# Kernel optimization log

Hardware: AMD Instinct MI355X
Metric: run time of the kernel (lower is better)

The kernel has to match this reference:

```python
import math
import jax, jax.numpy as jnp
from jax import lax
import numpy as np

N_LAYERS = 16
MAX_DIL = 128
C_RES = 64
C_DIL = 128
ENC_F = 256
ENC_S = 256
LOOP = int(math.floor(math.log2(MAX_DIL))) + 1  # 8
DILS = [2 ** (i % LOOP) for i in range(N_LAYERS)]  # 1..128 twice


def setup_inputs() -> dict:
    key = jax.random.key(0)
    ks = jax.random.split(key, 9)
    B, T = 8, 131072
    signal = jax.random.normal(ks[0], (B, 1, T), dtype=jnp.float32)
    # params (xavier-ish scales ~ 1/sqrt(fan_in+fan_out))
    W0 = jax.random.normal(ks[1], (C_RES, 1), dtype=jnp.float32) * 0.5          # 1x1 input conv
    b0 = jax.random.normal(ks[2], (C_RES,), dtype=jnp.float32) * 0.02
    Wd = jax.random.normal(ks[3], (N_LAYERS, C_DIL, C_RES, 2), dtype=jnp.float32) * 0.08  # k=2 dilated convs
    bd = jax.random.normal(ks[4], (N_LAYERS, C_DIL), dtype=jnp.float32) * 0.02
    Wr = jax.random.normal(ks[5], (N_LAYERS, C_RES, C_DIL), dtype=jnp.float32) * 0.08     # 1x1 residual convs
    br = jax.random.normal(ks[6], (N_LAYERS, C_RES), dtype=jnp.float32) * 0.02
    Wf = jax.random.normal(ks[7], (1, C_RES), dtype=jnp.float32) * 0.1          # 1x1 final conv
    bf = jax.random.normal(ks[8], (1,), dtype=jnp.float32) * 0.02
    return {"signal": signal, "W0": W0, "b0": b0, "Wd": Wd, "bd": bd,
            "Wr": Wr, "br": br, "Wf": Wf, "bf": bf}


def reference(signal, W0, b0, Wd, bd, Wr, br, Wf, bf):
    # input 1x1 conv: [B,1,T] -> [B,C_RES,T]
    x = jnp.einsum('oi,bit->bot', W0, signal) + b0[None, :, None]
    for i, d in enumerate(DILS):
        skip = x
        h = jax.nn.relu(x)
        # kernel-2 dilated conv, VALID (no causal pad in original): len shrinks by d
        L = h.shape[2]
        h = (jnp.einsum('oc,bct->bot', Wd[i, :, :, 0], h[:, :, :L - d])
             + jnp.einsum('oc,bct->bot', Wd[i, :, :, 1], h[:, :, d:])
             + bd[i][None, :, None])
        h = jax.nn.relu(h)
        # 1x1 residual conv back to C_RES
        h = jnp.einsum('oc,bct->bot', Wr[i], h) + br[i][None, :, None]
        # residual add with right-aligned trim of skip
        x = h + skip[:, :, skip.shape[2] - h.shape[2]:]
    # final 1x1 conv -> [B,1,L']
    x = jnp.einsum('oc,bct->bot', Wf, x) + bf[None, :, None]
    # AvgPool1d(ENC_F, stride=ENC_S), VALID, count_include_pad irrelevant (no pad)
    x = lax.reduce_window(x, 0.0, lax.add, (1, 1, ENC_F), (1, 1, ENC_S), 'VALID') / ENC_F
    return x
```

## Files before the change

kernel.cpp:

```cpp
#include <hip/hip_runtime.h>
#include <hip/hip_bf16.h>
#include <stdint.h>

typedef __attribute__((ext_vector_type(8))) short short8;
typedef __attribute__((ext_vector_type(4))) float f32x4;
typedef unsigned short bfu;

#define T_TILE  128
#define RING    384
#define NLAYERS 16
#define T0LEN   131072
#define BATCH   8
#define RFIELD  510
#define FINLEN  130560
#define CHCAP   65280

#define BARRIER() asm volatile("s_waitcnt lgkmcnt(0)\n\ts_barrier" ::: "memory")

__device__ __forceinline__ bfu f2bf(float f) {
    unsigned u = __float_as_uint(f);
    u += 0x7FFFu + ((u >> 16) & 1u);
    return (bfu)(u >> 16);
}
__device__ __forceinline__ unsigned pk2(float a, float b) {
    __hip_bfloat16 lo = __float2bfloat16(a);
    __hip_bfloat16 hi = __float2bfloat16(b);
    unsigned short ul = __builtin_bit_cast(unsigned short, lo);
    unsigned short uh = __builtin_bit_cast(unsigned short, hi);
    return (unsigned)ul | ((unsigned)uh << 16);
}
__device__ __forceinline__ float bf2f(bfu h) { return __uint_as_float(((unsigned)h) << 16); }
__device__ __forceinline__ unsigned relu2(unsigned w) {
    return w & ~(((w >> 15) & 0x00010001u) * 0xFFFFu);
}

__global__ void prep_weights(const float* __restrict__ Wd, const float* __restrict__ Wr,
                             bfu* __restrict__ wcat, bfu* __restrict__ wrb)
{
    int idx = blockIdx.x * 256 + threadIdx.x;
    const int total1 = NLAYERS * 128 * 128;
    if (idx < total1) {
        int k = idx & 127, o = (idx >> 7) & 127, l = idx >> 14;
        int tap = k >> 6, c = k & 63;
        wcat[idx] = f2bf(Wd[(((l * 128 + o) * 64) + c) * 2 + tap]);
    } else {
        int j = idx - total1;
        if (j < NLAYERS * 64 * 128) wrb[j] = f2bf(Wr[j]);
    }
}

template <int MODE>
__global__ __launch_bounds__(256, 2)
void layer_kernel(const bfu* __restrict__ xin, bfu* __restrict__ xout,
                  const bfu* __restrict__ wcat, const bfu* __restrict__ wrb,
                  const float* __restrict__ bd, const float* __restrict__ br,
                  const float* __restrict__ sig, const float* __restrict__ W0,
                  const float* __restrict__ b0, const float* __restrict__ Wf,
                  float* __restrict__ partial,
                  int s, int d, int Lin, int Lout, int Rrows, int NT, int tiles)
{
    __shared__ bfu rx[RING * 64];
    __shared__ bfu hb[128 * 128];

    const int tid  = threadIdx.x;
    const int lane = tid & 63;
    const int wv   = tid >> 6;
    const int l15  = lane & 15;
    const int lg   = lane >> 4;
    const int b    = blockIdx.y;

    const bfu* xb = xin  + (long)b * Rrows * 64;
    bfu*       xo = xout + (long)b * Rrows * 64;
    const float* sgb = sig + (long)b * T0LEN + s;

    short8 a1[2][4];
    #pragma unroll
    for (int m = 0; m < 2; ++m)
        #pragma unroll
        for (int k = 0; k < 4; ++k)
            a1[m][k] = *(const short8*)(wcat + ((wv * 32 + m * 16 + l15) << 7) + (k << 5) + (lg << 3));
    short8 a2[4];
    #pragma unroll
    for (int k = 0; k < 4; ++k)
        a2[k] = *(const short8*)(wrb + ((wv * 16 + l15) << 7) + (k << 5) + (lg << 3));

    const int c0 = wv * 16 + lg * 4;
    const f32x4 brv = *(const f32x4*)(br + c0);
    f32x4 bd4[2];
    #pragma unroll
    for (int m = 0; m < 2; ++m)
        bd4[m] = *(const f32x4*)(bd + wv * 32 + m * 16 + lg * 4);
    f32x4 wfv;
    if constexpr (MODE == 2) wfv = *(const f32x4*)(Wf + c0);

    const int tile0 = blockIdx.x * NT;
    const int jmax  = (tiles - tile0 < NT) ? (tiles - tile0) : NT;
    if (jmax <= 0) return;
    const int t00   = tile0 * T_TILE;

    if constexpr (MODE == 1) {
        const int nsl = (T_TILE + 1) * 8;
        #pragma unroll
        for (int it = 0; it < 5; ++it) {
            int i = tid + it * 256;
            if (i < nsl) {
                int r = i >> 3, oc = i & 7;
                int t = t00 + r; if (t > Lin - 1) t = Lin - 1;
                float sv = sgb[t];
                unsigned pk[4];
                #pragma unroll
                for (int kk = 0; kk < 4; ++kk) {
                    int c = oc * 8 + kk * 2;
                    pk[kk] = pk2(fmaxf(W0[c] * sv + b0[c], 0.f),
                                 fmaxf(W0[c + 1] * sv + b0[c + 1], 0.f));
                }
                int rs = (t00 + r) % RING;
                uint4 u; u.x = pk[0]; u.y = pk[1]; u.z = pk[2]; u.w = pk[3];
                *(uint4*)&rx[(rs << 6) + ((oc ^ (rs & 7)) << 3)] = u;
            }
        }
    } else {
        const int nsl = (T_TILE + d) * 8;
        uint4 pv[8];
        #pragma unroll
        for (int it = 0; it < 8; ++it) {
            int i = tid + it * 256;
            if (i < nsl) {
                int r = i >> 3, oc = i & 7;
                long t = t00 + r; if (t > Lin - 1) t = Lin - 1;
                pv[it] = *(const uint4*)(xb + t * 64 + oc * 8);
            }
        }
        #pragma unroll
        for (int it = 0; it < 8; ++it) {
            int i = tid + it * 256;
            if (i < nsl) {
                int r = i >> 3, oc = i & 7;
                int rs = (t00 + r) % RING;
                uint4 v = pv[it];
                v.x = relu2(v.x); v.y = relu2(v.y); v.z = relu2(v.z); v.w = relu2(v.w);
                *(uint4*)&rx[(rs << 6) + ((oc ^ (rs & 7)) << 3)] = v;
            }
        }
    }

    for (int j = 0; j < jmax; ++j) {
        const int t0    = t00 + j * T_TILE;
        const int base0 = t0 % RING;
        const int rbase = t0 + T_TILE + d;

        BARRIER();

        uint4 pf[4];
        float pfs[4];
        const bool havePF = (j + 1 < jmax);
        if (havePF) {
            if constexpr (MODE == 1) {
                #pragma unroll
                for (int it = 0; it < 4; ++it) {
                    int i = tid + it * 256;
                    int t = rbase + (i >> 3); if (t > Lin - 1) t = Lin - 1;
                    pfs[it] = sgb[t];
                }
            } else {
                #pragma unroll
                for (int it = 0; it < 4; ++it) {
                    int i = tid + it * 256;
                    int oc = i & 7;
                    long t = rbase + (i >> 3); if (t > Lin - 1) t = Lin - 1;
                    pf[it] = *(const uint4*)(xb + t * 64 + oc * 8);
                }
            }
        }

        uint2 sk[8];
        float skv[8];
        if constexpr (MODE == 1) {
            #pragma unroll
            for (int n = 0; n < 8; ++n) {
                int t = t0 + n * 16 + l15;
                skv[n] = (t < Lout) ? sgb[t + d] : 0.f;
            }
        } else {
            #pragma unroll
            for (int n = 0; n < 8; ++n) {
                int t = t0 + n * 16 + l15;
                uint2 z = {0u, 0u};
                sk[n] = (t < Lout) ? *(const uint2*)(xb + (long)(t + d) * 64 + c0) : z;
            }
        }

        f32x4 acc[2][8];
        #pragma unroll
        for (int m = 0; m < 2; ++m)
            #pragma unroll
            for (int n = 0; n < 8; ++n) acc[m][n] = bd4[m];
        __builtin_amdgcn_s_setprio(1);
        #pragma unroll
        for (int k = 0; k < 4; ++k) {
            const int roff = (k >> 1) ? d : 0;
            const int g    = ((k & 1) << 2) + lg;
            #pragma unroll
            for (int n = 0; n < 8; ++n) {
                int rr = base0 + n * 16 + l15 + roff;
                if (rr >= RING) rr -= RING;
                short8 bv = *(const short8*)&rx[(rr << 6) + ((g ^ (rr & 7)) << 3)];
                acc[0][n] = __builtin_amdgcn_mfma_f32_16x16x32_bf16(a1[0][k], bv, acc[0][n], 0, 0, 0);
                acc[1][n] = __builtin_amdgcn_mfma_f32_16x16x32_bf16(a1[1][k], bv, acc[1][n], 0, 0, 0);
            }
        }
        __builtin_amdgcn_s_setprio(0);

        #pragma unroll
        for (int m = 0; m < 2; ++m) {
            const int o0 = wv * 32 + m * 16 + lg * 4;
            const int gg = o0 >> 3;
            #pragma unroll
            for (int n = 0; n < 8; ++n) {
                int t = n * 16 + l15;
                f32x4 h = acc[m][n];
                unsigned q01 = pk2(fmaxf(h.x, 0.f), fmaxf(h.y, 0.f));
                unsigned q23 = pk2(fmaxf(h.z, 0.f), fmaxf(h.w, 0.f));
                int idx = (t << 7) + (((gg ^ (t & 15)) << 3) | (o0 & 7));
                uint2 pk; pk.x = q01; pk.y = q23;
                *(uint2*)&hb[idx] = pk;
            }
        }

        if (havePF) {
            if constexpr (MODE == 1) {
                #pragma unroll
                for (int it = 0; it < 4; ++it) {
                    int i = tid + it * 256;
                    int r = i >> 3, oc = i & 7;
                    float sv = pfs[it];
                    unsigned pk[4];
                    #pragma unroll
                    for (int kk = 0; kk < 4; ++kk) {
                        int c = oc * 8 + kk * 2;
                        pk[kk] = pk2(fmaxf(W0[c] * sv + b0[c], 0.f),
                                     fmaxf(W0[c + 1] * sv + b0[c + 1], 0.f));
                    }
                    int rs = (rbase + r) % RING;
                    uint4 u; u.x = pk[0]; u.y = pk[1]; u.z = pk[2]; u.w = pk[3];
                    *(uint4*)&rx[(rs << 6) + ((oc ^ (rs & 7)) << 3)] = u;
                }
            } else {
                #pragma unroll
                for (int it = 0; it < 4; ++it) {
                    int i = tid + it * 256;
                    int r = i >> 3, oc = i & 7;
                    int rs = (rbase + r) % RING;
                    uint4 v = pf[it];
                    v.x = relu2(v.x); v.y = relu2(v.y); v.z = relu2(v.z); v.w = relu2(v.w);
                    *(uint4*)&rx[(rs << 6) + ((oc ^ (rs & 7)) << 3)] = v;
                }
            }
        }

        BARRIER();

        f32x4 acc2[8];
        #pragma unroll
        for (int n = 0; n < 8; ++n) acc2[n] = brv;
        __builtin_amdgcn_s_setprio(1);
        #pragma unroll
        for (int k = 0; k < 4; ++k) {
            const int g = (k << 2) + lg;
            #pragma unroll
            for (int n = 0; n < 8; ++n) {
                int t = n * 16 + l15;
                short8 bfm = *(const short8*)&hb[(t << 7) + ((g ^ (t & 15)) << 3)];
                acc2[n] = __builtin_amdgcn_mfma_f32_16x16x32_bf16(a2[k], bfm, acc2[n], 0, 0, 0);
            }
        }
        __builtin_amdgcn_s_setprio(0);

        float psum = 0.f;
        #pragma unroll
        for (int n = 0; n < 8; ++n) {
            int t = t0 + n * 16 + l15;
            if (t < Lout) {
                float s0, s1, s2, s3;
                if constexpr (MODE == 1) {
                    float sv = skv[n];
                    s0 = W0[c0] * sv + b0[c0];         s1 = W0[c0 + 1] * sv + b0[c0 + 1];
                    s2 = W0[c0 + 2] * sv + b0[c0 + 2]; s3 = W0[c0 + 3] * sv + b0[c0 + 3];
                } else {
                    s0 = bf2f((bfu)(sk[n].x & 0xFFFF)); s1 = bf2f((bfu)(sk[n].x >> 16));
                    s2 = bf2f((bfu)(sk[n].y & 0xFFFF)); s3 = bf2f((bfu)(sk[n].y >> 16));
                }
                float y0 = acc2[n].x + s0;
                float y1 = acc2[n].y + s1;
                float y2 = acc2[n].z + s2;
                float y3 = acc2[n].w + s3;
                if constexpr (MODE == 2) {
                    psum += wfv.x * y0 + wfv.y * y1 + wfv.z * y2 + wfv.w * y3;
                } else {
                    uint2 pk;
                    pk.x = pk2(y0, y1);
                    pk.y = pk2(y2, y3);
                    *(uint2*)(xo + (long)t * 64 + c0) = pk;
                }
            }
        }
        if constexpr (MODE == 2) {
            #pragma unroll
            for (int off = 32; off > 0; off >>= 1) psum += __shfl_down(psum, off, 64);
            if (lane == 0)
                partial[((long)b * 1024 + ((s + t0) >> 7)) * 4 + wv] = psum;
        }
    }
}

__global__ void pool_reduce(const float* __restrict__ part, const float* __restrict__ bfp,
                            float* __restrict__ out)
{
    int i = blockIdx.x * 256 + threadIdx.x;
    if (i >= BATCH * 510) return;
    int b = i / 510, w = i % 510;
    const float* p = part + ((long)b * 1024 + 2 * w) * 4;
    float sum = p[0] + p[1] + p[2] + p[3] + p[4] + p[5] + p[6] + p[7];
    out[i] = sum * (1.0f / 256.0f) + bfp[0];
}

extern "C" void kernel_launch(void* const* d_in, const int* in_sizes, int n_in,
                              void* d_out, int out_size, void* d_ws, size_t ws_size,
                              hipStream_t stream) {
    const float* sig = (const float*)d_in[0];
    const float* W0  = (const float*)d_in[1];
    const float* b0  = (const float*)d_in[2];
    const float* Wd  = (const float*)d_in[3];
    const float* bd  = (const float*)d_in[4];
    const float* Wr  = (const float*)d_in[5];
    const float* br  = (const float*)d_in[6];
    const float* Wf  = (const float*)d_in[7];
    const float* bf  = (const float*)d_in[8];
    float* out = (float*)d_out;

    char* ws = (char*)d_ws;
    const size_t WCAT_E = (size_t)NLAYERS * 128 * 128;
    const size_t WRB_E  = (size_t)NLAYERS * 64 * 128;
    const size_t WBYTES = (WCAT_E + WRB_E) * 2;
    const size_t PARTB  = (size_t)BATCH * 1024 * 4 * 4;
    bfu*   wcat    = (bfu*)ws;
    bfu*   wrb     = (bfu*)(ws + WCAT_E * 2);
    float* partial = (float*)(ws + WBYTES);

    if (ws_size < WBYTES + PARTB + (size_t)2 * BATCH * 766 * 64 * 2) return;

    size_t avail   = ws_size - WBYTES - PARTB;
    long   rowsMax = (long)(avail / ((size_t)2 * BATCH * 64 * 2));
    long   CH      = ((rowsMax - RFIELD) / 256) * 256;
    if (CH > CHCAP) CH = CHCAP;
    if (CH < 256)   CH = 256;
    const long Rrows = CH + RFIELD;

    bfu* xA = (bfu*)(ws + WBYTES + PARTB);
    bfu* xB = xA + (size_t)BATCH * Rrows * 64;

    const int totw = (int)(WCAT_E + WRB_E);
    prep_weights<<<(totw + 255) / 256, 256, 0, stream>>>(Wd, Wr, wcat, wrb);

    bfu* bufs[2] = {xA, xB};
    for (long s = 0; s < FINLEN; s += CH) {
        long CHc  = (FINLEN - s < CH) ? (FINLEN - s) : CH;
        int  len0 = (int)(CHc + RFIELD);

        int cur = 0;
        int L = len0;
        for (int i = 0; i < NLAYERS; ++i) {
            int d = 1 << (i & 7);
            int Lout = L - d;
            int tiles = (Lout + T_TILE - 1) / T_TILE;
            int NT    = (tiles + 63) / 64;
            int bx    = (tiles + NT - 1) / NT;
            dim3 grid(bx, BATCH);
            const bfu* xi = bufs[cur];
            bfu*       xo = bufs[cur ^ 1];
            const bfu* wc  = wcat + (size_t)i * 128 * 128;
            const bfu* wr2 = wrb  + (size_t)i * 64 * 128;
            const float* bdl = bd + i * 128;
            const float* brl = br + i * 64;
            if (i == 0)
                layer_kernel<1><<<grid, 256, 0, stream>>>(xi, xo, wc, wr2, bdl, brl,
                    sig, W0, b0, Wf, partial, (int)s, d, L, Lout, (int)Rrows, NT, tiles);
            else if (i == NLAYERS - 1)
                layer_kernel<2><<<grid, 256, 0, stream>>>(xi, xo, wc, wr2, bdl, brl,
                    sig, W0, b0, Wf, partial, (int)s, d, L, Lout, (int)Rrows, NT, tiles);
            else
                layer_kernel<0><<<grid, 256, 0, stream>>>(xi, xo, wc, wr2, bdl, brl,
                    sig, W0, b0, Wf, partial, (int)s, d, L, Lout, (int)Rrows, NT, tiles);
            cur ^= 1;
            L = Lout;
        }
    }
    pool_reduce<<<(BATCH * 510 + 255) / 256, 256, 0, stream>>>(partial, bf, out);
}
```

Baseline: 1.663 ms.

## Split waves 2x2 over channels and time to raise MFMA operand reuse

Each of the four waves used to own a slice of output channels across all 128 time steps of the tile. Now the waves form a 2x2 grid: channel half (ow) by time half (tw). Each shared-memory B fragment read now feeds 4 MFMAs in the dilated conv GEMM instead of 2, and 2 instead of 1 in the residual GEMM, cutting LDS read traffic per MFMA. The W0/b0 skip weights are also loaded once into registers. In exchange each wave keeps more weight fragments and accumulators live, which raises VGPR pressure.

```diff
diff --git a/kernel.cpp b/kernel.cpp
--- a/kernel.cpp
+++ b/kernel.cpp
@@ -65,6 +65,8 @@
     const int tid  = threadIdx.x;
     const int lane = tid & 63;
     const int wv   = tid >> 6;
+    const int ow   = wv & 1;
+    const int tw   = wv >> 1;
     const int l15  = lane & 15;
     const int lg   = lane >> 4;
     const int b    = blockIdx.y;
@@ -73,25 +75,31 @@
     bfu*       xo = xout + (long)b * Rrows * 64;
     const float* sgb = sig + (long)b * T0LEN + s;
 
-    short8 a1[2][4];
+    short8 a1[4][4];
+    #pragma unroll
+    for (int m = 0; m < 4; ++m)
+        #pragma unroll
+        for (int k = 0; k < 4; ++k)
+            a1[m][k] = *(const short8*)(wcat + ((ow * 64 + m * 16 + l15) << 7) + (k << 5) + (lg << 3));
+    short8 a2[2][4];
     #pragma unroll
     for (int m = 0; m < 2; ++m)
         #pragma unroll
         for (int k = 0; k < 4; ++k)
-            a1[m][k] = *(const short8*)(wcat + ((wv * 32 + m * 16 + l15) << 7) + (k << 5) + (lg << 3));
-    short8 a2[4];
+            a2[m][k] = *(const short8*)(wrb + ((ow * 32 + m * 16 + l15) << 7) + (k << 5) + (lg << 3));
+
+    f32x4 bd4[4];
     #pragma unroll
-    for (int k = 0; k < 4; ++k)
-        a2[k] = *(const short8*)(wrb + ((wv * 16 + l15) << 7) + (k << 5) + (lg << 3));
-
-    const int c0 = wv * 16 + lg * 4;
-    const f32x4 brv = *(const f32x4*)(br + c0);
-    f32x4 bd4[2];
+    for (int m = 0; m < 4; ++m)
+        bd4[m] = *(const f32x4*)(bd + ow * 64 + m * 16 + lg * 4);
+    f32x4 brv[2], wfv[2], w0v[2], b0v[2];
     #pragma unroll
-    for (int m = 0; m < 2; ++m)
-        bd4[m] = *(const f32x4*)(bd + wv * 32 + m * 16 + lg * 4);
-    f32x4 wfv;
-    if constexpr (MODE == 2) wfv = *(const f32x4*)(Wf + c0);
+    for (int m = 0; m < 2; ++m) {
+        int c0m = ow * 32 + m * 16 + lg * 4;
+        brv[m] = *(const f32x4*)(br + c0m);
+        if constexpr (MODE == 2) wfv[m] = *(const f32x4*)(Wf + c0m);
+        if constexpr (MODE == 1) { w0v[m] = *(const f32x4*)(W0 + c0m); b0v[m] = *(const f32x4*)(b0 + c0m); }
+    }
 
     const int tile0 = blockIdx.x * NT;
     const int jmax  = (tiles - tile0 < NT) ? (tiles - tile0) : NT;
@@ -173,51 +181,57 @@
             }
         }
 
-        uint2 sk[8];
-        float skv[8];
+        uint2 sk[2][4];
+        float skv[4];
         if constexpr (MODE == 1) {
             #pragma unroll
-            for (int n = 0; n < 8; ++n) {
-                int t = t0 + n * 16 + l15;
+            for (int n = 0; n < 4; ++n) {
+                int t = t0 + tw * 64 + n * 16 + l15;
                 skv[n] = (t < Lout) ? sgb[t + d] : 0.f;
             }
         } else {
             #pragma unroll
-            for (int n = 0; n < 8; ++n) {
-                int t = t0 + n * 16 + l15;
-                uint2 z = {0u, 0u};
-                sk[n] = (t < Lout) ? *(const uint2*)(xb + (long)(t + d) * 64 + c0) : z;
-            }
-        }
-
-        f32x4 acc[2][8];
-        #pragma unroll
-        for (int m = 0; m < 2; ++m)
-            #pragma unroll
-            for (int n = 0; n < 8; ++n) acc[m][n] = bd4[m];
+            for (int m = 0; m < 2; ++m) {
+                int c0m = ow * 32 + m * 16 + lg * 4;
+                #pragma unroll
+                for (int n = 0; n < 4; ++n) {
+                    int t = t0 + tw * 64 + n * 16 + l15;
+                    uint2 z = {0u, 0u};
+                    sk[m][n] = (t < Lout) ? *(const uint2*)(xb + (long)(t + d) * 64 + c0m) : z;
+                }
+            }
+        }
+
+        f32x4 acc[4][4];
+        #pragma unroll
+        for (int m = 0; m < 4; ++m)
+            #pragma unroll
+            for (int n = 0; n < 4; ++n) acc[m][n] = bd4[m];
         __builtin_amdgcn_s_setprio(1);
         #pragma unroll
         for (int k = 0; k < 4; ++k) {
             const int roff = (k >> 1) ? d : 0;
             const int g    = ((k & 1) << 2) + lg;
             #pragma unroll
-            for (int n = 0; n < 8; ++n) {
-                int rr = base0 + n * 16 + l15 + roff;
+            for (int n = 0; n < 4; ++n) {
+                int rr = base0 + tw * 64 + n * 16 + l15 + roff;
                 if (rr >= RING) rr -= RING;
                 short8 bv = *(const short8*)&rx[(rr << 6) + ((g ^ (rr & 7)) << 3)];
                 acc[0][n] = __builtin_amdgcn_mfma_f32_16x16x32_bf16(a1[0][k], bv, acc[0][n], 0, 0, 0);
                 acc[1][n] = __builtin_amdgcn_mfma_f32_16x16x32_bf16(a1[1][k], bv, acc[1][n], 0, 0, 0);
+                acc[2][n] = __builtin_amdgcn_mfma_f32_16x16x32_bf16(a1[2][k], bv, acc[2][n], 0, 0, 0);
+                acc[3][n] = __builtin_amdgcn_mfma_f32_16x16x32_bf16(a1[3][k], bv, acc[3][n], 0, 0, 0);
             }
         }
         __builtin_amdgcn_s_setprio(0);
 
         #pragma unroll
-        for (int m = 0; m < 2; ++m) {
-            const int o0 = wv * 32 + m * 16 + lg * 4;
+        for (int m = 0; m < 4; ++m) {
+            const int o0 = ow * 64 + m * 16 + lg * 4;
             const int gg = o0 >> 3;
             #pragma unroll
-            for (int n = 0; n < 8; ++n) {
-                int t = n * 16 + l15;
+            for (int n = 0; n < 4; ++n) {
+                int t = tw * 64 + n * 16 + l15;
                 f32x4 h = acc[m][n];
                 unsigned q01 = pk2(fmaxf(h.x, 0.f), fmaxf(h.y, 0.f));
                 unsigned q23 = pk2(fmaxf(h.z, 0.f), fmaxf(h.w, 0.f));
@@ -260,47 +274,54 @@
 
         BARRIER();
 
-        f32x4 acc2[8];
-        #pragma unroll
-        for (int n = 0; n < 8; ++n) acc2[n] = brv;
+        f32x4 acc2[2][4];
+        #pragma unroll
+        for (int m = 0; m < 2; ++m)
+            #pragma unroll
+            for (int n = 0; n < 4; ++n) acc2[m][n] = brv[m];
         __builtin_amdgcn_s_setprio(1);
         #pragma unroll
         for (int k = 0; k < 4; ++k) {
             const int g = (k << 2) + lg;
             #pragma unroll
-            for (int n = 0; n < 8; ++n) {
-                int t = n * 16 + l15;
+            for (int n = 0; n < 4; ++n) {
+                int t = tw * 64 + n * 16 + l15;
                 short8 bfm = *(const short8*)&hb[(t << 7) + ((g ^ (t & 15)) << 3)];
-                acc2[n] = __builtin_amdgcn_mfma_f32_16x16x32_bf16(a2[k], bfm, acc2[n], 0, 0, 0);
+                acc2[0][n] = __builtin_amdgcn_mfma_f32_16x16x32_bf16(a2[0][k], bfm, acc2[0][n], 0, 0, 0);
+                acc2[1][n] = __builtin_amdgcn_mfma_f32_16x16x32_bf16(a2[1][k], bfm, acc2[1][n], 0, 0, 0);
             }
         }
         __builtin_amdgcn_s_setprio(0);
 
         float psum = 0.f;
         #pragma unroll
-        for (int n = 0; n < 8; ++n) {
-            int t = t0 + n * 16 + l15;
-            if (t < Lout) {
-                float s0, s1, s2, s3;
-                if constexpr (MODE == 1) {
-                    float sv = skv[n];
-                    s0 = W0[c0] * sv + b0[c0];         s1 = W0[c0 + 1] * sv + b0[c0 + 1];
-                    s2 = W0[c0 + 2] * sv + b0[c0 + 2]; s3 = W0[c0 + 3] * sv + b0[c0 + 3];
-                } else {
-                    s0 = bf2f((bfu)(sk[n].x & 0xFFFF)); s1 = bf2f((bfu)(sk[n].x >> 16));
-                    s2 = bf2f((bfu)(sk[n].y & 0xFFFF)); s3 = bf2f((bfu)(sk[n].y >> 16));
-                }
-                float y0 = acc2[n].x + s0;
-                float y1 = acc2[n].y + s1;
-                float y2 = acc2[n].z + s2;
-                float y3 = acc2[n].w + s3;
-                if constexpr (MODE == 2) {
-                    psum += wfv.x * y0 + wfv.y * y1 + wfv.z * y2 + wfv.w * y3;
-                } else {
-                    uint2 pk;
-                    pk.x = pk2(y0, y1);
-                    pk.y = pk2(y2, y3);
-                    *(uint2*)(xo + (long)t * 64 + c0) = pk;
+        for (int m = 0; m < 2; ++m) {
+            const int c0m = ow * 32 + m * 16 + lg * 4;
+            #pragma unroll
+            for (int n = 0; n < 4; ++n) {
+                int t = t0 + tw * 64 + n * 16 + l15;
+                if (t < Lout) {
+                    float s0, s1, s2, s3;
+                    if constexpr (MODE == 1) {
+                        float sv = skv[n];
+                        s0 = w0v[m].x * sv + b0v[m].x;  s1 = w0v[m].y * sv + b0v[m].y;
+                        s2 = w0v[m].z * sv + b0v[m].z;  s3 = w0v[m].w * sv + b0v[m].w;
+                    } else {
+                        s0 = bf2f((bfu)(sk[m][n].x & 0xFFFF)); s1 = bf2f((bfu)(sk[m][n].x >> 16));
+                        s2 = bf2f((bfu)(sk[m][n].y & 0xFFFF)); s3 = bf2f((bfu)(sk[m][n].y >> 16));
+                    }
+                    float y0 = acc2[m][n].x + s0;
+                    float y1 = acc2[m][n].y + s1;
+                    float y2 = acc2[m][n].z + s2;
+                    float y3 = acc2[m][n].w + s3;
+                    if constexpr (MODE == 2) {
+                        psum += wfv[m].x * y0 + wfv[m].y * y1 + wfv[m].z * y2 + wfv[m].w * y3;
+                    } else {
+                        uint2 pk;
+                        pk.x = pk2(y0, y1);
+                        pk.y = pk2(y2, y3);
+                        *(uint2*)(xo + (long)t * 64 + c0m) = pk;
+                    }
                 }
             }
         }
```

Result: slower. 1.936 ms (+16.4%).

## Run both time chunks concurrently in one launch per layer via grid z

Applied to the files above, without the earlier changes.

When the time axis splits into exactly two chunks and the workspace can hold four activation buffers, both chunks are processed together: each layer is launched once with a z dimension of 2, and each z slice gets its own buffer pair and time offset. The tiles handled per block are halved so each launch has more blocks. This halves the number of kernel launches and serial layer dependencies and raises occupancy per launch, in exchange for doubling the activation workspace footprint. If the condition fails, the old sequential chunk loop is kept.

```diff
diff --git a/kernel.cpp b/kernel.cpp
--- a/kernel.cpp
+++ b/kernel.cpp
@@ -57,7 +57,8 @@
                   const float* __restrict__ sig, const float* __restrict__ W0,
                   const float* __restrict__ b0, const float* __restrict__ Wf,
                   float* __restrict__ partial,
-                  int s, int d, int Lin, int Lout, int Rrows, int NT, int tiles)
+                  int s, int d, int Lin, int Lout, int Rrows, int NT, int tiles,
+                  int chunkCH, long chunkElems)
 {
     __shared__ bfu rx[RING * 64];
     __shared__ bfu hb[128 * 128];
@@ -68,6 +69,11 @@
     const int l15  = lane & 15;
     const int lg   = lane >> 4;
     const int b    = blockIdx.y;
+    const int zc   = blockIdx.z;
+
+    s += zc * chunkCH;
+    xin  += (size_t)zc * chunkElems;
+    xout += (size_t)zc * chunkElems;
 
     const bfu* xb = xin  + (long)b * Rrows * 64;
     bfu*       xo = xout + (long)b * Rrows * 64;
@@ -355,27 +361,29 @@
     if (CH > CHCAP) CH = CHCAP;
     if (CH < 256)   CH = 256;
     const long Rrows = CH + RFIELD;
-
-    bfu* xA = (bfu*)(ws + WBYTES + PARTB);
-    bfu* xB = xA + (size_t)BATCH * Rrows * 64;
+    const long E       = (long)BATCH * Rrows * 64;
+    const size_t BUFB  = (size_t)E * 2;
+
+    const bool merged = (FINLEN == 2 * CH) &&
+                        (ws_size >= WBYTES + PARTB + 4 * BUFB);
 
     const int totw = (int)(WCAT_E + WRB_E);
     prep_weights<<<(totw + 255) / 256, 256, 0, stream>>>(Wd, Wr, wcat, wrb);
 
-    bfu* bufs[2] = {xA, xB};
-    for (long s = 0; s < FINLEN; s += CH) {
-        long CHc  = (FINLEN - s < CH) ? (FINLEN - s) : CH;
-        int  len0 = (int)(CHc + RFIELD);
-
+    if (merged) {
+        bfu* xA = (bfu*)(ws + WBYTES + PARTB);
+        bfu* xB = xA + 2 * E;
+        bfu* bufs[2] = {xA, xB};
         int cur = 0;
+        int len0 = (int)(CH + RFIELD);
         int L = len0;
         for (int i = 0; i < NLAYERS; ++i) {
             int d = 1 << (i & 7);
             int Lout = L - d;
             int tiles = (Lout + T_TILE - 1) / T_TILE;
-            int NT    = (tiles + 63) / 64;
+            int NT    = (tiles + 31) / 32;
             int bx    = (tiles + NT - 1) / NT;
-            dim3 grid(bx, BATCH);
+            dim3 grid(bx, BATCH, 2);
             const bfu* xi = bufs[cur];
             bfu*       xo = bufs[cur ^ 1];
             const bfu* wc  = wcat + (size_t)i * 128 * 128;
@@ -384,16 +392,57 @@
             const float* brl = br + i * 64;
             if (i == 0)
                 layer_kernel<1><<<grid, 256, 0, stream>>>(xi, xo, wc, wr2, bdl, brl,
-                    sig, W0, b0, Wf, partial, (int)s, d, L, Lout, (int)Rrows, NT, tiles);
+                    sig, W0, b0, Wf, partial, 0, d, L, Lout, (int)Rrows, NT, tiles,
+                    (int)CH, E);
             else if (i == NLAYERS - 1)
                 layer_kernel<2><<<grid, 256, 0, stream>>>(xi, xo, wc, wr2, bdl, brl,
-                    sig, W0, b0, Wf, partial, (int)s, d, L, Lout, (int)Rrows, NT, tiles);
+                    sig, W0, b0, Wf, partial, 0, d, L, Lout, (int)Rrows, NT, tiles,
+                    (int)CH, E);
             else
                 layer_kernel<0><<<grid, 256, 0, stream>>>(xi, xo, wc, wr2, bdl, brl,
-                    sig, W0, b0, Wf, partial, (int)s, d, L, Lout, (int)Rrows, NT, tiles);
+                    sig, W0, b0, Wf, partial, 0, d, L, Lout, (int)Rrows, NT, tiles,
+                    (int)CH, E);
             cur ^= 1;
             L = Lout;
         }
+    } else {
+        bfu* xA = (bfu*)(ws + WBYTES + PARTB);
+        bfu* xB = xA + E;
+        bfu* bufs[2] = {xA, xB};
+        for (long s = 0; s < FINLEN; s += CH) {
+            long CHc  = (FINLEN - s < CH) ? (FINLEN - s) : CH;
+            int  len0 = (int)(CHc + RFIELD);
+            int cur = 0;
+            int L = len0;
+            for (int i = 0; i < NLAYERS; ++i) {
+                int d = 1 << (i & 7);
+                int Lout = L - d;
+                int tiles = (Lout + T_TILE - 1) / T_TILE;
+                int NT    = (tiles + 63) / 64;
+                int bx    = (tiles + NT - 1) / NT;
+                dim3 grid(bx, BATCH);
+                const bfu* xi = bufs[cur];
+                bfu*       xo = bufs[cur ^ 1];
+                const bfu* wc  = wcat + (size_t)i * 128 * 128;
+                const bfu* wr2 = wrb  + (size_t)i * 64 * 128;
+                const float* bdl = bd + i * 128;
+                const float* brl = br + i * 64;
+                if (i == 0)
+                    layer_kernel<1><<<grid, 256, 0, stream>>>(xi, xo, wc, wr2, bdl, brl,
+                        sig, W0, b0, Wf, partial, (int)s, d, L, Lout, (int)Rrows, NT, tiles,
+                        0, 0);
+                else if (i == NLAYERS - 1)
+                    layer_kernel<2><<<grid, 256, 0, stream>>>(xi, xo, wc, wr2, bdl, brl,
+                        sig, W0, b0, Wf, partial, (int)s, d, L, Lout, (int)Rrows, NT, tiles,
+                        0, 0);
+                else
+                    layer_kernel<0><<<grid, 256, 0, stream>>>(xi, xo, wc, wr2, bdl, brl,
+                        sig, W0, b0, Wf, partial, (int)s, d, L, Lout, (int)Rrows, NT, tiles,
+                        0, 0);
+                cur ^= 1;
+                L = Lout;
+            }
+        }
     }
     pool_reduce<<<(BATCH * 510 + 255) / 256, 256, 0, stream>>>(partial, bf, out);
 }
```

Measured after the change: 1.663 ms. About the same (-0.0%).
